# Performance work log

Hardware: AMD Instinct MI355X
Metric: run time of the kernel (lower is better)

Reference implementation:

```python
import jax, jax.numpy as jnp
import numpy as np

B, S, D, H = 2, 2048, 1024, 16
DH = D // H
DFF = 4 * D
EPS = 1e-5
NEG = -1e9


def _layernorm(x, gamma, beta):
    mu = jnp.mean(x, axis=-1, keepdims=True)
    var = jnp.mean(jnp.square(x - mu), axis=-1, keepdims=True)
    return (x - mu) * jax.lax.rsqrt(var + EPS) * gamma + beta


def setup_inputs() -> dict:
    key = jax.random.key(0)
    ks = jax.random.split(key, 12)
    s = 0.02
    X = jax.random.normal(ks[0], (B, S, D), dtype=jnp.float32)
    # causal mask (True = attend)
    attention_mask = jnp.tril(jnp.ones((S, S), dtype=bool))
    return {
        "X": X,
        "attention_mask": attention_mask,
        "gamma1": jnp.ones((D,), jnp.float32),
        "beta1": jnp.zeros((D,), jnp.float32),
        "Wq": jax.random.normal(ks[1], (H, D, DH), jnp.float32) * s,
        "bq": jnp.zeros((H, DH), jnp.float32),
        "Wk": jax.random.normal(ks[2], (H, D, DH), jnp.float32) * s,
        "bk": jnp.zeros((H, DH), jnp.float32),
        "Wv": jax.random.normal(ks[3], (H, D, DH), jnp.float32) * s,
        "bv": jnp.zeros((H, DH), jnp.float32),
        "W0": jax.random.normal(ks[4], (D, D), jnp.float32) * s,
        "b0": jnp.zeros((D,), jnp.float32),
        "gamma2": jnp.ones((D,), jnp.float32),
        "beta2": jnp.zeros((D,), jnp.float32),
        "W1": jax.random.normal(ks[5], (D, DFF), jnp.float32) * s,
        "b1": jnp.zeros((DFF,), jnp.float32),
        "W2": jax.random.normal(ks[6], (DFF, D), jnp.float32) * s,
        "b2": jnp.zeros((D,), jnp.float32),
    }


def reference(X, attention_mask, gamma1, beta1, Wq, bq, Wk, bk, Wv, bv, W0, b0,
              gamma2, beta2, W1, b1, W2, b2):
    scale = 1.0 / np.sqrt(DH)
    # --- pre-LN MHA ---
    Xn = _layernorm(X, gamma1, beta1)
    # per-head projections, stacked: [B,H,S,DH]
    Q = jnp.einsum('bsd,hdk->bhsk', Xn, Wq) + bq[None, :, None, :]
    K = jnp.einsum('bsd,hdk->bhsk', Xn, Wk) + bk[None, :, None, :]
    V = jnp.einsum('bsd,hdk->bhsk', Xn, Wv) + bv[None, :, None, :]
    scores = jnp.einsum('bhsk,bhtk->bhst', Q, K) * scale
    scores = jnp.where(attention_mask, scores, NEG)
    weights = jax.nn.softmax(scores, axis=-1)
    attn = jnp.einsum('bhst,bhtv->bhsv', weights, V)  # [B,H,S,DH]
    # concat heads (head-major along feature dim, matching torch.cat order)
    attn = attn.transpose(0, 2, 1, 3).reshape(B, S, D)
    mha = attn @ W0 + b0
    X = mha + X  # residual (dropout = identity at eval)
    # --- pre-LN FFN ---
    Xn2 = _layernorm(X, gamma2, beta2)
    h = jax.nn.relu(Xn2 @ W1 + b1)
    ffn = h @ W2 + b2
    return ffn + X
```

## Files before the change

### kernel.cpp

```cpp
#include <hip/hip_runtime.h>
#include <hip/hip_bf16.h>

#define BB 2
#define SS 2048
#define DDIM 1024
#define HH 16
#define DHH 64
#define DFF_ 4096
#define BS 4096
#define NQKV 3072

typedef unsigned short u16;
using short8  = __attribute__((ext_vector_type(8))) short;
using floatx4 = __attribute__((ext_vector_type(4))) float;
using ushort4_t = __attribute__((ext_vector_type(4))) unsigned short;

__device__ __forceinline__ u16 f2b(float f){
  union { unsigned int u; float f; } v; v.f = f;
  unsigned int u = v.u;
  u += 0x7FFFu + ((u >> 16) & 1u);
  return (u16)(u >> 16);
}

__device__ __forceinline__ void gl2lds16(const u16* g, u16* l){
  __builtin_amdgcn_global_load_lds((const __attribute__((address_space(1))) void*)g,
                                   (__attribute__((address_space(3))) void*)l, 16, 0, 0);
}

__device__ __forceinline__ void ln_row(const float* __restrict__ x,
                                       const float* __restrict__ gamma,
                                       const float* __restrict__ beta,
                                       u16* __restrict__ y, int row, float* smem){
  const float4* xr = (const float4*)(x + (size_t)row * DDIM);
  int tid = threadIdx.x;
  float4 v = xr[tid];
  float s  = v.x + v.y + v.z + v.w;
  float ss = v.x*v.x + v.y*v.y + v.z*v.z + v.w*v.w;
  for (int o = 1; o < 64; o <<= 1){ s += __shfl_xor(s, o, 64); ss += __shfl_xor(ss, o, 64); }
  int wid = tid >> 6;
  if ((tid & 63) == 0){ smem[wid] = s; smem[wid + 4] = ss; }
  __syncthreads();
  s  = smem[0] + smem[1] + smem[2] + smem[3];
  ss = smem[4] + smem[5] + smem[6] + smem[7];
  float mu  = s / (float)DDIM;
  float var = ss / (float)DDIM - mu * mu;
  float rs  = rsqrtf(var + 1e-5f);
  const float4* gp = (const float4*)gamma;
  const float4* bp = (const float4*)beta;
  float4 g = gp[tid], b = bp[tid];
  u16* yr = y + (size_t)row * DDIM + tid*4;
  yr[0] = f2b((v.x - mu) * rs * g.x + b.x);
  yr[1] = f2b((v.y - mu) * rs * g.y + b.y);
  yr[2] = f2b((v.z - mu) * rs * g.z + b.z);
  yr[3] = f2b((v.w - mu) * rs * g.w + b.w);
}

__device__ __forceinline__ void tcast(const float* __restrict__ in, u16* __restrict__ out,
                                      int R, int C, int tile, float (*sh)[33]){
  int nr = R >> 5;
  int tr = tile % nr, tc = tile / nr;
  int r0 = tr * 32, c0 = tc * 32;
  int tx = threadIdx.x & 31, ty = threadIdx.x >> 5;
  for (int i = ty; i < 32; i += 8)
    sh[i][tx] = in[(size_t)(r0 + i) * C + c0 + tx];
  __syncthreads();
  for (int i = ty; i < 32; i += 8)
    out[(size_t)(c0 + i) * R + r0 + tx] = f2b(sh[tx][i]);
}

__global__ __launch_bounds__(256) void prep_ln1_k(
    const float* __restrict__ X, const float* __restrict__ g1, const float* __restrict__ be1,
    u16* __restrict__ Xn,
    const float* __restrict__ Wq, const float* __restrict__ Wk, const float* __restrict__ Wv,
    const float* __restrict__ W0, const float* __restrict__ W1,
    const float* __restrict__ bq, const float* __restrict__ bk, const float* __restrict__ bv,
    u16* __restrict__ wqkvT, u16* __restrict__ w0T, u16* __restrict__ w1T,
    float* __restrict__ biasQKV)
{
  __shared__ float sh[32][33];
  __shared__ float smem8[8];
  int id = blockIdx.x;
  if (id < 4096){
    ln_row(X, g1, be1, Xn, id, smem8);
  } else if (id < 7168){
    int lid2 = id - 4096;
    int which = lid2 >> 10, lid = lid2 & 1023;
    const float* src = which == 0 ? Wq : (which == 1 ? Wk : Wv);
    u16* dst = wqkvT + (size_t)which * 1048576;
    int bat = lid >> 6, t = lid & 63;
    tcast(src + (size_t)bat * 65536, dst + (size_t)bat * 65536, 1024, 64, t, sh);
  } else if (id < 8192){
    tcast(W0, w0T, 1024, 1024, id - 7168, sh);
  } else if (id < 12288){
    tcast(W1, w1T, 1024, 4096, id - 8192, sh);
  } else {
    int idx = (id - 12288) * 256 + threadIdx.x;
    if (idx < 3072){
      float v = idx < 1024 ? bq[idx] : (idx < 2048 ? bk[idx - 1024] : bv[idx - 2048]);
      biasQKV[idx] = v;
    }
  }
}

__global__ __launch_bounds__(256) void w2t_ln2_k(
    const float* __restrict__ X1, const float* __restrict__ g2, const float* __restrict__ be2,
    u16* __restrict__ Xn2, const float* __restrict__ W2, u16* __restrict__ w2T)
{
  __shared__ float sh[32][33];
  __shared__ float smem8[8];
  int id = blockIdx.x;
  if (id < 4096){
    ln_row(X1, g2, be2, Xn2, id, smem8);
  } else {
    int tile = id - 4096;
    int tr = tile / 32, tc = tile % 32;
    int r0 = tr * 32, c0 = tc * 32;
    int tx = threadIdx.x & 31, ty = threadIdx.x >> 5;
    for (int i = ty; i < 32; i += 8)
      sh[i][tx] = W2[(size_t)(r0 + i) * 1024 + c0 + tx];
    __syncthreads();
    for (int i = ty; i < 32; i += 8)
      w2T[(size_t)(c0 + i) * 4096 + r0 + tx] = f2b(sh[tx][i]);
  }
}

__global__ __launch_bounds__(256) void vt_k(const u16* __restrict__ QKV, u16* __restrict__ VT){
  __shared__ u16 t[32][33];
  int bh = blockIdx.z; int b = bh >> 4, h = bh & 15;
  int s0 = blockIdx.x * 32, d0 = blockIdx.y * 32;
  int tx = threadIdx.x & 31, ty = threadIdx.x >> 5;
  const u16* src = QKV + (size_t)b * SS * NQKV + 2048 + h * DHH;
  for (int i = ty; i < 32; i += 8)
    t[i][tx] = src[(size_t)(s0 + i) * NQKV + d0 + tx];
  __syncthreads();
  u16* dst = VT + (size_t)bh * DHH * SS;
  for (int i = ty; i < 32; i += 8)
    dst[(size_t)(d0 + i) * SS + s0 + tx] = t[tx][i];
}

template<int TM, int TN>
__global__ __launch_bounds__(256) void gemm_db(
    const u16* __restrict__ A, const u16* __restrict__ Bt,
    const float* __restrict__ bias, const float* __restrict__ res,
    void* __restrict__ Cv, int M, int N, int K, int relu, int writeBf16)
{
  constexpr int ACH = TM / 16;
  constexpr int BCH = TN / 16;
  constexpr int CH1 = ACH + BCH;
  constexpr int CPW = (2 * CH1) / 4;
  constexpr int MI  = TM / 32;
  constexpr int NI  = TN / 32;

  __shared__ __align__(16) u16 As[2][2][TM * 32];
  __shared__ __align__(16) u16 Bs[2][2][TN * 32];

  int tid  = threadIdx.x;
  int wave = tid >> 6, lane = tid & 63;
  int quad = lane >> 4, l16 = lane & 15;

  int gx = gridDim.x, gy = gridDim.y;
  int bid = blockIdx.x + gx * blockIdx.y;
  int xcd = bid & 7, idx = bid >> 3;
  int by  = xcd * (gy >> 3) + idx / gx;
  int bx  = idx % gx;

  int m0 = by * TM, n0 = bx * TN;
  int wm = (wave >> 1) * (TM / 2), wn = (wave & 1) * (TN / 2);

  floatx4 acc[MI][NI] = {};

  int srow = lane >> 2;
  int scol = (lane & 3) * 8;
  const u16* gptr[CPW]; u16* lp0[CPW]; int lstep[CPW];
#pragma unroll
  for (int k = 0; k < CPW; k++){
    int c = wave * CPW + k;
    int p = c / CH1, cc = c % CH1;
    if (cc < ACH){
      gptr[k]  = A + (size_t)(m0 + cc*16 + srow) * K + p*32 + scol;
      lp0[k]   = &As[0][p][cc * 512];
      lstep[k] = 2 * TM * 32;
    } else {
      gptr[k]  = Bt + (size_t)(n0 + (cc-ACH)*16 + srow) * K + p*32 + scol;
      lp0[k]   = &Bs[0][p][(cc-ACH) * 512];
      lstep[k] = 2 * TN * 32;
    }
  }

  int nsteps = K >> 6;

#pragma unroll
  for (int k = 0; k < CPW; k++){ gl2lds16(gptr[k], lp0[k]); gptr[k] += 64; }
  asm volatile("s_waitcnt vmcnt(0)" ::: "memory");
  __builtin_amdgcn_sched_barrier(0);
  __builtin_amdgcn_s_barrier();
  __builtin_amdgcn_sched_barrier(0);

  for (int t = 0; t < nsteps; ++t){
    int cur = t & 1;
    if (t + 1 < nsteps){
#pragma unroll
      for (int k = 0; k < CPW; k++){
        gl2lds16(gptr[k], lp0[k] + (cur ? 0 : lstep[k]));
        gptr[k] += 64;
      }
    }
    __builtin_amdgcn_s_setprio(1);
#pragma unroll
    for (int p = 0; p < 2; p++){
      short8 af[MI], bf[NI];
#pragma unroll
      for (int i = 0; i < MI; i++)
        af[i] = *(short8*)&As[cur][p][(wm + i*16 + l16)*32 + quad*8];
#pragma unroll
      for (int j = 0; j < NI; j++)
        bf[j] = *(short8*)&Bs[cur][p][(wn + j*16 + l16)*32 + quad*8];
#pragma unroll
      for (int i = 0; i < MI; i++)
#pragma unroll
        for (int j = 0; j < NI; j++)
          acc[i][j] = __builtin_amdgcn_mfma_f32_16x16x32_bf16(bf[j], af[i], acc[i][j], 0,0,0);
    }
    __builtin_amdgcn_s_setprio(0);
    if (t + 1 < nsteps){
      asm volatile("s_waitcnt vmcnt(0)" ::: "memory");
      __builtin_amdgcn_sched_barrier(0);
      __builtin_amdgcn_s_barrier();
      __builtin_amdgcn_sched_barrier(0);
    }
  }

  u16*   Cb = (u16*)Cv;
  float* Cf = (float*)Cv;
#pragma unroll
  for (int i = 0; i < MI; i++){
    int row = m0 + wm + i*16 + l16;
#pragma unroll
    for (int j = 0; j < NI; j++){
      int col = n0 + wn + j*16 + quad*4;
      float v0 = acc[i][j][0], v1 = acc[i][j][1], v2 = acc[i][j][2], v3 = acc[i][j][3];
      if (bias){
        const float4 bb = *(const float4*)&bias[col];
        v0 += bb.x; v1 += bb.y; v2 += bb.z; v3 += bb.w;
      }
      if (relu){
        v0 = v0 > 0.f ? v0 : 0.f; v1 = v1 > 0.f ? v1 : 0.f;
        v2 = v2 > 0.f ? v2 : 0.f; v3 = v3 > 0.f ? v3 : 0.f;
      }
      if (res){
        const float4 rr = *(const float4*)&res[(size_t)row * N + col];
        v0 += rr.x; v1 += rr.y; v2 += rr.z; v3 += rr.w;
      }
      if (writeBf16){
        ushort4_t o = { f2b(v0), f2b(v1), f2b(v2), f2b(v3) };
        *(ushort4_t*)&Cb[(size_t)row * N + col] = o;
      } else {
        float4 o; o.x = v0; o.y = v1; o.z = v2; o.w = v3;
        *(float4*)&Cf[(size_t)row * N + col] = o;
      }
    }
  }
}

#define KT   128
#define KsLD 72
#define VTLD 136
#define PsLD 136

__global__ __launch_bounds__(256) void attn_k(
    const u16* __restrict__ QKV, const u16* __restrict__ VT, u16* __restrict__ O)
{
  int bh = blockIdx.x;
  int b = bh >> 4, h = bh & 15;
  int qt = (int)gridDim.y - 1 - blockIdx.y;
  int q0 = qt * 64;
  const u16* Qb_  = QKV + (size_t)b * SS * NQKV + h * DHH;
  const u16* Kb_  = Qb_ + 1024;
  const u16* VTb_ = VT + (size_t)bh * DHH * SS;

  __shared__ __align__(16) u16 Ks [KT * KsLD];
  __shared__ __align__(16) u16 VTs[DHH * VTLD];
  __shared__ __align__(16) u16 Ps [4][16 * PsLD];

  int tid = threadIdx.x;
  int wave = tid >> 6, lane = tid & 63;
  int quad = lane >> 4, l16 = lane & 15;
  int qrow = q0 + wave * 16;

  short8 qf0, qf1;
  {
    const u16* qp = Qb_ + (size_t)(qrow + l16) * NQKV + quad*8;
    qf0 = *(const short8*)qp;
    qf1 = *(const short8*)(qp + 32);
  }

  float l_acc[4] = {0.f, 0.f, 0.f, 0.f};
  floatx4 oacc[4] = {};

  int nk = (qt >> 1) + 1;
  int lim = wave + 4 * (qt & 1);
  const float qs = 0.125f * 1.44269504088896f;

  short8 kreg[4], vreg[4];
#pragma unroll
  for (int it = 0; it < 4; it++){
    int g = tid + it * 256;
    kreg[it] = *(const short8*)(Kb_ + (size_t)(g >> 3) * NQKV + (g & 7) * 8);
    vreg[it] = *(const short8*)(VTb_ + (size_t)(g >> 4) * SS + (g & 15) * 8);
  }

  for (int kt = 0; kt < nk; kt++){
    int k0 = kt * KT;
    __syncthreads();
#pragma unroll
    for (int it = 0; it < 4; it++){
      int g = tid + it * 256;
      *(short8*)&Ks [(g >> 3) * KsLD + (g & 7) * 8]  = kreg[it];
      *(short8*)&VTs[(g >> 4) * VTLD + (g & 15) * 8] = vreg[it];
    }
    __syncthreads();

    if (kt + 1 < nk){
      int kn = k0 + KT;
#pragma unroll
      for (int it = 0; it < 4; it++){
        int g = tid + it * 256;
        kreg[it] = *(const short8*)(Kb_ + (size_t)(kn + (g >> 3)) * NQKV + (g & 7) * 8);
        vreg[it] = *(const short8*)(VTb_ + (size_t)(g >> 4) * SS + kn + (g & 15) * 8);
      }
    }

    bool last = (kt == nk - 1);
    int stmax = last ? lim : 7;
    floatx4 sacc[8] = {};
    __builtin_amdgcn_s_setprio(1);
#pragma unroll
    for (int st = 0; st < 8; st++){
      if (st <= stmax){
        short8 kb0 = *(short8*)&Ks[(st*16 + l16) * KsLD + quad*8];
        short8 kb1 = *(short8*)&Ks[(st*16 + l16) * KsLD + 32 + quad*8];
        sacc[st] = __builtin_amdgcn_mfma_f32_16x16x32_bf16(qf0, kb0, sacc[st], 0,0,0);
        sacc[st] = __builtin_amdgcn_mfma_f32_16x16x32_bf16(qf1, kb1, sacc[st], 0,0,0);
      }
    }
    __builtin_amdgcn_s_setprio(0);

#pragma unroll
    for (int st = 0; st < 8; st++){
      if (st <= stmax){
        if (last){
          int col = k0 + st*16 + l16;
#pragma unroll
          for (int r = 0; r < 4; r++){
            float e = exp2f(sacc[st][r] * qs);
            e = (col <= qrow + quad*4 + r) ? e : 0.f;
            l_acc[r] += e;
            Ps[wave][(quad*4 + r) * PsLD + st*16 + l16] = f2b(e);
          }
        } else {
#pragma unroll
          for (int r = 0; r < 4; r++){
            float e = exp2f(sacc[st][r] * qs);
            l_acc[r] += e;
            Ps[wave][(quad*4 + r) * PsLD + st*16 + l16] = f2b(e);
          }
        }
      } else {
#pragma unroll
        for (int r = 0; r < 4; r++)
          Ps[wave][(quad*4 + r) * PsLD + st*16 + l16] = 0;
      }
    }
    asm volatile("s_waitcnt lgkmcnt(0)" ::: "memory");

    int cmax = last ? (lim >> 1) : 3;
    short8 pa[4];
#pragma unroll
    for (int c = 0; c < 4; c++)
      pa[c] = *(short8*)&Ps[wave][l16 * PsLD + c*32 + quad*8];
    __builtin_amdgcn_s_setprio(1);
#pragma unroll
    for (int ost = 0; ost < 4; ost++){
#pragma unroll
      for (int c = 0; c < 4; c++){
        if (c <= cmax){
          short8 vb = *(short8*)&VTs[(ost*16 + l16) * VTLD + c*32 + quad*8];
          oacc[ost] = __builtin_amdgcn_mfma_f32_16x16x32_bf16(pa[c], vb, oacc[ost], 0,0,0);
        }
      }
    }
    __builtin_amdgcn_s_setprio(0);
  }

#pragma unroll
  for (int r = 0; r < 4; r++){
    for (int o = 1; o < 16; o <<= 1) l_acc[r] += __shfl_xor(l_acc[r], o, 64);
  }
  float inv[4];
#pragma unroll
  for (int r = 0; r < 4; r++) inv[r] = 1.0f / l_acc[r];

#pragma unroll
  for (int ost = 0; ost < 4; ost++)
#pragma unroll
    for (int r = 0; r < 4; r++){
      int s  = qrow + quad*4 + r;
      int dh = ost*16 + l16;
      O[((size_t)b * SS + s) * DDIM + h * DHH + dh] = f2b(oacc[ost][r] * inv[r]);
    }
}

extern "C" void kernel_launch(void* const* d_in, const int* in_sizes, int n_in,
                              void* d_out, int out_size, void* d_ws, size_t ws_size,
                              hipStream_t stream) {
  const float* X   = (const float*)d_in[0];
  const float* g1  = (const float*)d_in[2];
  const float* be1 = (const float*)d_in[3];
  const float* Wq  = (const float*)d_in[4];
  const float* bq  = (const float*)d_in[5];
  const float* Wk  = (const float*)d_in[6];
  const float* bk  = (const float*)d_in[7];
  const float* Wv  = (const float*)d_in[8];
  const float* bv  = (const float*)d_in[9];
  const float* W0  = (const float*)d_in[10];
  const float* b0  = (const float*)d_in[11];
  const float* g2  = (const float*)d_in[12];
  const float* be2 = (const float*)d_in[13];
  const float* W1  = (const float*)d_in[14];
  const float* b1  = (const float*)d_in[15];
  const float* W2  = (const float*)d_in[16];
  const float* b2  = (const float*)d_in[17];
  float* out = (float*)d_out;

  u16* ws16 = (u16*)d_ws;
  u16* wqkvT = ws16;
  u16* w0T   = ws16 + 3145728;
  u16* w2T   = ws16;
  u16* w1T   = ws16 + 4194304;
  u16* QKVb  = ws16 + 8388608;
  u16* VTb   = ws16 + 8388608 + 12582912;
  u16* hb    = ws16 + 8388608;
  u16* Xn    = ws16 + 25165824;
  u16* attnB = Xn;
  float* biasQKV = (float*)(ws16 + 29360128);

  prep_ln1_k<<<dim3(12300), 256, 0, stream>>>(X, g1, be1, Xn,
      Wq, Wk, Wv, W0, W1, bq, bk, bv, wqkvT, w0T, w1T, biasQKV);

  gemm_db<128,128><<<dim3(24, 32), 256, 0, stream>>>(Xn, wqkvT, biasQKV, nullptr, QKVb,
      BS, NQKV, 1024, 0, 1);

  vt_k<<<dim3(64, 2, 32), 256, 0, stream>>>(QKVb, VTb);

  attn_k<<<dim3(32, 32), 256, 0, stream>>>(QKVb, VTb, attnB);

  gemm_db<64,128><<<dim3(8, 64), 256, 0, stream>>>(attnB, w0T, b0, X, out,
      BS, DDIM, 1024, 0, 0);

  w2t_ln2_k<<<dim3(8192), 256, 0, stream>>>(out, g2, be2, Xn, W2, w2T);

  gemm_db<128,128><<<dim3(32, 32), 256, 0, stream>>>(Xn, w1T, b1, nullptr, hb,
      BS, DFF_, 1024, 1, 1);
  gemm_db<64,128><<<dim3(8, 64), 256, 0, stream>>>(hb, w2T, b2, out, out,
      BS, DDIM, DFF_, 0, 0);
}
```

Measured before the change: 370.2 us.

## Process 128 query rows per attention block to reuse K/V tiles

Each attention block now handles two 64-row query groups per wave pair (128 rows), sharing each staged K and V^T tile across both groups, and the grid is halved. This cuts global K/V loads and LDS staging per query row. In exchange, register pressure from doubled score and output accumulators rises, and fewer blocks with uneven causal work may reduce occupancy and load balance.

```diff
diff --git a/kernel.cpp b/kernel.cpp
--- a/kernel.cpp
+++ b/kernel.cpp
@@ -273,7 +273,7 @@
   int bh = blockIdx.x;
   int b = bh >> 4, h = bh & 15;
   int qt = (int)gridDim.y - 1 - blockIdx.y;
-  int q0 = qt * 64;
+  int q0 = qt * 128;
   const u16* Qb_  = QKV + (size_t)b * SS * NQKV + h * DHH;
   const u16* Kb_  = Qb_ + 1024;
   const u16* VTb_ = VT + (size_t)bh * DHH * SS;
@@ -285,20 +285,25 @@
   int tid = threadIdx.x;
   int wave = tid >> 6, lane = tid & 63;
   int quad = lane >> 4, l16 = lane & 15;
-  int qrow = q0 + wave * 16;
-
-  short8 qf0, qf1;
+  int qrow0 = q0 + wave * 16;
+  int qrow1 = qrow0 + 64;
+
+  short8 qf0a, qf0b, qf1a, qf1b;
   {
-    const u16* qp = Qb_ + (size_t)(qrow + l16) * NQKV + quad*8;
-    qf0 = *(const short8*)qp;
-    qf1 = *(const short8*)(qp + 32);
-  }
-
-  float l_acc[4] = {0.f, 0.f, 0.f, 0.f};
-  floatx4 oacc[4] = {};
-
-  int nk = (qt >> 1) + 1;
-  int lim = wave + 4 * (qt & 1);
+    const u16* qp0 = Qb_ + (size_t)(qrow0 + l16) * NQKV + quad*8;
+    qf0a = *(const short8*)qp0;
+    qf0b = *(const short8*)(qp0 + 32);
+    const u16* qp1 = Qb_ + (size_t)(qrow1 + l16) * NQKV + quad*8;
+    qf1a = *(const short8*)qp1;
+    qf1b = *(const short8*)(qp1 + 32);
+  }
+
+  float l0[4] = {0.f,0.f,0.f,0.f}, l1[4] = {0.f,0.f,0.f,0.f};
+  floatx4 oa0[4] = {}, oa1[4] = {};
+
+  int nk = qt + 1;
+  int lim0 = wave;
+  int lim1 = wave + 4;
   const float qs = 0.125f * 1.44269504088896f;
 
   short8 kreg[4], vreg[4];
@@ -331,37 +336,43 @@
     }
 
     bool last = (kt == nk - 1);
-    int stmax = last ? lim : 7;
-    floatx4 sacc[8] = {};
+    int s0max = last ? lim0 : 7;
+    int s1max = last ? lim1 : 7;
+
+    floatx4 sacc0[8] = {}, sacc1[8] = {};
     __builtin_amdgcn_s_setprio(1);
 #pragma unroll
     for (int st = 0; st < 8; st++){
-      if (st <= stmax){
+      if (st <= s1max){
         short8 kb0 = *(short8*)&Ks[(st*16 + l16) * KsLD + quad*8];
         short8 kb1 = *(short8*)&Ks[(st*16 + l16) * KsLD + 32 + quad*8];
-        sacc[st] = __builtin_amdgcn_mfma_f32_16x16x32_bf16(qf0, kb0, sacc[st], 0,0,0);
-        sacc[st] = __builtin_amdgcn_mfma_f32_16x16x32_bf16(qf1, kb1, sacc[st], 0,0,0);
+        if (st <= s0max){
+          sacc0[st] = __builtin_amdgcn_mfma_f32_16x16x32_bf16(qf0a, kb0, sacc0[st], 0,0,0);
+          sacc0[st] = __builtin_amdgcn_mfma_f32_16x16x32_bf16(qf0b, kb1, sacc0[st], 0,0,0);
+        }
+        sacc1[st] = __builtin_amdgcn_mfma_f32_16x16x32_bf16(qf1a, kb0, sacc1[st], 0,0,0);
+        sacc1[st] = __builtin_amdgcn_mfma_f32_16x16x32_bf16(qf1b, kb1, sacc1[st], 0,0,0);
       }
     }
     __builtin_amdgcn_s_setprio(0);
 
 #pragma unroll
     for (int st = 0; st < 8; st++){
-      if (st <= stmax){
+      if (st <= s0max){
         if (last){
           int col = k0 + st*16 + l16;
 #pragma unroll
           for (int r = 0; r < 4; r++){
-            float e = exp2f(sacc[st][r] * qs);
-            e = (col <= qrow + quad*4 + r) ? e : 0.f;
-            l_acc[r] += e;
+            float e = exp2f(sacc0[st][r] * qs);
+            e = (col <= qrow0 + quad*4 + r) ? e : 0.f;
+            l0[r] += e;
             Ps[wave][(quad*4 + r) * PsLD + st*16 + l16] = f2b(e);
           }
         } else {
 #pragma unroll
           for (int r = 0; r < 4; r++){
-            float e = exp2f(sacc[st][r] * qs);
-            l_acc[r] += e;
+            float e = exp2f(sacc0[st][r] * qs);
+            l0[r] += e;
             Ps[wave][(quad*4 + r) * PsLD + st*16 + l16] = f2b(e);
           }
         }
@@ -373,40 +384,95 @@
     }
     asm volatile("s_waitcnt lgkmcnt(0)" ::: "memory");
 
-    int cmax = last ? (lim >> 1) : 3;
-    short8 pa[4];
-#pragma unroll
-    for (int c = 0; c < 4; c++)
-      pa[c] = *(short8*)&Ps[wave][l16 * PsLD + c*32 + quad*8];
-    __builtin_amdgcn_s_setprio(1);
-#pragma unroll
-    for (int ost = 0; ost < 4; ost++){
-#pragma unroll
-      for (int c = 0; c < 4; c++){
-        if (c <= cmax){
-          short8 vb = *(short8*)&VTs[(ost*16 + l16) * VTLD + c*32 + quad*8];
-          oacc[ost] = __builtin_amdgcn_mfma_f32_16x16x32_bf16(pa[c], vb, oacc[ost], 0,0,0);
+    {
+      int cmax = last ? (lim0 >> 1) : 3;
+      short8 pa[4];
+#pragma unroll
+      for (int c = 0; c < 4; c++)
+        pa[c] = *(short8*)&Ps[wave][l16 * PsLD + c*32 + quad*8];
+      __builtin_amdgcn_s_setprio(1);
+#pragma unroll
+      for (int ost = 0; ost < 4; ost++){
+#pragma unroll
+        for (int c = 0; c < 4; c++){
+          if (c <= cmax){
+            short8 vb = *(short8*)&VTs[(ost*16 + l16) * VTLD + c*32 + quad*8];
+            oa0[ost] = __builtin_amdgcn_mfma_f32_16x16x32_bf16(pa[c], vb, oa0[ost], 0,0,0);
+          }
         }
       }
-    }
-    __builtin_amdgcn_s_setprio(0);
+      __builtin_amdgcn_s_setprio(0);
+    }
+
+#pragma unroll
+    for (int st = 0; st < 8; st++){
+      if (st <= s1max){
+        if (last){
+          int col = k0 + st*16 + l16;
+#pragma unroll
+          for (int r = 0; r < 4; r++){
+            float e = exp2f(sacc1[st][r] * qs);
+            e = (col <= qrow1 + quad*4 + r) ? e : 0.f;
+            l1[r] += e;
+            Ps[wave][(quad*4 + r) * PsLD + st*16 + l16] = f2b(e);
+          }
+        } else {
+#pragma unroll
+          for (int r = 0; r < 4; r++){
+            float e = exp2f(sacc1[st][r] * qs);
+            l1[r] += e;
+            Ps[wave][(quad*4 + r) * PsLD + st*16 + l16] = f2b(e);
+          }
+        }
+      } else {
+#pragma unroll
+        for (int r = 0; r < 4; r++)
+          Ps[wave][(quad*4 + r) * PsLD + st*16 + l16] = 0;
+      }
+    }
+    asm volatile("s_waitcnt lgkmcnt(0)" ::: "memory");
+
+    {
+      int cmax = last ? (lim1 >> 1) : 3;
+      short8 pa[4];
+#pragma unroll
+      for (int c = 0; c < 4; c++)
+        pa[c] = *(short8*)&Ps[wave][l16 * PsLD + c*32 + quad*8];
+      __builtin_amdgcn_s_setprio(1);
+#pragma unroll
+      for (int ost = 0; ost < 4; ost++){
+#pragma unroll
+        for (int c = 0; c < 4; c++){
+          if (c <= cmax){
+            short8 vb = *(short8*)&VTs[(ost*16 + l16) * VTLD + c*32 + quad*8];
+            oa1[ost] = __builtin_amdgcn_mfma_f32_16x16x32_bf16(pa[c], vb, oa1[ost], 0,0,0);
+          }
+        }
+      }
+      __builtin_amdgcn_s_setprio(0);
+    }
   }
 
 #pragma unroll
   for (int r = 0; r < 4; r++){
-    for (int o = 1; o < 16; o <<= 1) l_acc[r] += __shfl_xor(l_acc[r], o, 64);
-  }
-  float inv[4];
-#pragma unroll
-  for (int r = 0; r < 4; r++) inv[r] = 1.0f / l_acc[r];
+    for (int o = 1; o < 16; o <<= 1){
+      l0[r] += __shfl_xor(l0[r], o, 64);
+      l1[r] += __shfl_xor(l1[r], o, 64);
+    }
+  }
+  float inv0[4], inv1[4];
+#pragma unroll
+  for (int r = 0; r < 4; r++){ inv0[r] = 1.0f / l0[r]; inv1[r] = 1.0f / l1[r]; }
 
 #pragma unroll
   for (int ost = 0; ost < 4; ost++)
 #pragma unroll
     for (int r = 0; r < 4; r++){
-      int s  = qrow + quad*4 + r;
       int dh = ost*16 + l16;
-      O[((size_t)b * SS + s) * DDIM + h * DHH + dh] = f2b(oacc[ost][r] * inv[r]);
+      int s0r = qrow0 + quad*4 + r;
+      int s1r = qrow1 + quad*4 + r;
+      O[((size_t)b * SS + s0r) * DDIM + h * DHH + dh] = f2b(oa0[ost][r] * inv0[r]);
+      O[((size_t)b * SS + s1r) * DDIM + h * DHH + dh] = f2b(oa1[ost][r] * inv1[r]);
     }
 }
 
@@ -452,7 +518,7 @@
 
   vt_k<<<dim3(64, 2, 32), 256, 0, stream>>>(QKVb, VTb);
 
-  attn_k<<<dim3(32, 32), 256, 0, stream>>>(QKVb, VTb, attnB);
+  attn_k<<<dim3(32, 16), 256, 0, stream>>>(QKVb, VTb, attnB);
 
   gemm_db<64,128><<<dim3(8, 64), 256, 0, stream>>>(attnB, w0T, b0, X, out,
       BS, DDIM, 1024, 0, 0);
```

After: 411.8 us. +11.2%, slower.

## Double attention block to 128 query rows and swizzle LDS layouts

Applied to the files above, without the earlier changes.

The attention kernel now runs 512 threads (8 waves) per block covering 128 query rows instead of 64. Each K/V tile loaded into LDS is therefore shared by twice as many waves, halving the number of blocks and the per-block global loads. The padded LDS strides are replaced with XOR-swizzled unpadded layouts for K, V^T and P, meant to avoid bank conflicts. The trade-off is fewer blocks in the grid, so the causal load imbalance per block gets coarser.

```diff
diff --git a/kernel.cpp b/kernel.cpp
--- a/kernel.cpp
+++ b/kernel.cpp
@@ -262,30 +262,27 @@
   }
 }
 
-#define KT   128
-#define KsLD 72
-#define VTLD 136
-#define PsLD 136
-
-__global__ __launch_bounds__(256) void attn_k(
+#define KT 128
+
+__global__ __launch_bounds__(512) void attn_k(
     const u16* __restrict__ QKV, const u16* __restrict__ VT, u16* __restrict__ O)
 {
   int bh = blockIdx.x;
   int b = bh >> 4, h = bh & 15;
-  int qt = (int)gridDim.y - 1 - blockIdx.y;
-  int q0 = qt * 64;
+  int t  = (int)gridDim.y - 1 - blockIdx.y;
   const u16* Qb_  = QKV + (size_t)b * SS * NQKV + h * DHH;
   const u16* Kb_  = Qb_ + 1024;
   const u16* VTb_ = VT + (size_t)bh * DHH * SS;
 
-  __shared__ __align__(16) u16 Ks [KT * KsLD];
-  __shared__ __align__(16) u16 VTs[DHH * VTLD];
-  __shared__ __align__(16) u16 Ps [4][16 * PsLD];
+  __shared__ __align__(16) u16 Ks [KT * 64];
+  __shared__ __align__(16) u16 VTs[DHH * 128];
+  __shared__ __align__(16) u16 Ps [8][16 * 128];
 
   int tid = threadIdx.x;
   int wave = tid >> 6, lane = tid & 63;
+  int g = wave >> 2, w = wave & 3;
   int quad = lane >> 4, l16 = lane & 15;
-  int qrow = q0 + wave * 16;
+  int qrow = t * 128 + g * 64 + w * 16;
 
   short8 qf0, qf1;
   {
@@ -297,36 +294,38 @@
   float l_acc[4] = {0.f, 0.f, 0.f, 0.f};
   floatx4 oacc[4] = {};
 
-  int nk = (qt >> 1) + 1;
-  int lim = wave + 4 * (qt & 1);
+  int nk = t + 1;
+  int lim = w + 4 * g;
   const float qs = 0.125f * 1.44269504088896f;
 
-  short8 kreg[4], vreg[4];
-#pragma unroll
-  for (int it = 0; it < 4; it++){
-    int g = tid + it * 256;
-    kreg[it] = *(const short8*)(Kb_ + (size_t)(g >> 3) * NQKV + (g & 7) * 8);
-    vreg[it] = *(const short8*)(VTb_ + (size_t)(g >> 4) * SS + (g & 15) * 8);
+  short8 kreg[2], vreg[2];
+#pragma unroll
+  for (int it = 0; it < 2; it++){
+    int gg = tid + it * 512;
+    kreg[it] = *(const short8*)(Kb_ + (size_t)(gg >> 3) * NQKV + (gg & 7) * 8);
+    vreg[it] = *(const short8*)(VTb_ + (size_t)(gg >> 4) * SS + (gg & 15) * 8);
   }
 
   for (int kt = 0; kt < nk; kt++){
     int k0 = kt * KT;
     __syncthreads();
 #pragma unroll
-    for (int it = 0; it < 4; it++){
-      int g = tid + it * 256;
-      *(short8*)&Ks [(g >> 3) * KsLD + (g & 7) * 8]  = kreg[it];
-      *(short8*)&VTs[(g >> 4) * VTLD + (g & 15) * 8] = vreg[it];
+    for (int it = 0; it < 2; it++){
+      int gg = tid + it * 512;
+      { int row = gg >> 3, idx = (row * 64 + (gg & 7) * 8) ^ ((row & 7) << 3);
+        *(short8*)&Ks[idx] = kreg[it]; }
+      { int row = gg >> 4, idx = (row * 128 + (gg & 15) * 8) ^ ((row & 7) << 3);
+        *(short8*)&VTs[idx] = vreg[it]; }
     }
     __syncthreads();
 
     if (kt + 1 < nk){
       int kn = k0 + KT;
 #pragma unroll
-      for (int it = 0; it < 4; it++){
-        int g = tid + it * 256;
-        kreg[it] = *(const short8*)(Kb_ + (size_t)(kn + (g >> 3)) * NQKV + (g & 7) * 8);
-        vreg[it] = *(const short8*)(VTb_ + (size_t)(g >> 4) * SS + kn + (g & 15) * 8);
+      for (int it = 0; it < 2; it++){
+        int gg = tid + it * 512;
+        kreg[it] = *(const short8*)(Kb_ + (size_t)(kn + (gg >> 3)) * NQKV + (gg & 7) * 8);
+        vreg[it] = *(const short8*)(VTb_ + (size_t)(gg >> 4) * SS + kn + (gg & 15) * 8);
       }
     }
 
@@ -337,8 +336,10 @@
 #pragma unroll
     for (int st = 0; st < 8; st++){
       if (st <= stmax){
-        short8 kb0 = *(short8*)&Ks[(st*16 + l16) * KsLD + quad*8];
-        short8 kb1 = *(short8*)&Ks[(st*16 + l16) * KsLD + 32 + quad*8];
+        int r0i = (st*16 + l16) * 64;
+        int sw  = (l16 & 7) << 3;
+        short8 kb0 = *(short8*)&Ks[(r0i + quad*8) ^ sw];
+        short8 kb1 = *(short8*)&Ks[(r0i + 32 + quad*8) ^ sw];
         sacc[st] = __builtin_amdgcn_mfma_f32_16x16x32_bf16(qf0, kb0, sacc[st], 0,0,0);
         sacc[st] = __builtin_amdgcn_mfma_f32_16x16x32_bf16(qf1, kb1, sacc[st], 0,0,0);
       }
@@ -355,20 +356,24 @@
             float e = exp2f(sacc[st][r] * qs);
             e = (col <= qrow + quad*4 + r) ? e : 0.f;
             l_acc[r] += e;
-            Ps[wave][(quad*4 + r) * PsLD + st*16 + l16] = f2b(e);
+            int row = quad*4 + r;
+            Ps[wave][(row * 128 + st*16 + l16) ^ ((row & 7) << 3)] = f2b(e);
           }
         } else {
 #pragma unroll
           for (int r = 0; r < 4; r++){
             float e = exp2f(sacc[st][r] * qs);
             l_acc[r] += e;
-            Ps[wave][(quad*4 + r) * PsLD + st*16 + l16] = f2b(e);
+            int row = quad*4 + r;
+            Ps[wave][(row * 128 + st*16 + l16) ^ ((row & 7) << 3)] = f2b(e);
           }
         }
       } else {
 #pragma unroll
-        for (int r = 0; r < 4; r++)
-          Ps[wave][(quad*4 + r) * PsLD + st*16 + l16] = 0;
+        for (int r = 0; r < 4; r++){
+          int row = quad*4 + r;
+          Ps[wave][(row * 128 + st*16 + l16) ^ ((row & 7) << 3)] = 0;
+        }
       }
     }
     asm volatile("s_waitcnt lgkmcnt(0)" ::: "memory");
@@ -377,14 +382,14 @@
     short8 pa[4];
 #pragma unroll
     for (int c = 0; c < 4; c++)
-      pa[c] = *(short8*)&Ps[wave][l16 * PsLD + c*32 + quad*8];
+      pa[c] = *(short8*)&Ps[wave][(l16 * 128 + c*32 + quad*8) ^ ((l16 & 7) << 3)];
     __builtin_amdgcn_s_setprio(1);
 #pragma unroll
     for (int ost = 0; ost < 4; ost++){
 #pragma unroll
       for (int c = 0; c < 4; c++){
         if (c <= cmax){
-          short8 vb = *(short8*)&VTs[(ost*16 + l16) * VTLD + c*32 + quad*8];
+          short8 vb = *(short8*)&VTs[((ost*16 + l16) * 128 + c*32 + quad*8) ^ ((l16 & 7) << 3)];
           oacc[ost] = __builtin_amdgcn_mfma_f32_16x16x32_bf16(pa[c], vb, oacc[ost], 0,0,0);
         }
       }
@@ -452,7 +457,7 @@
 
   vt_k<<<dim3(64, 2, 32), 256, 0, stream>>>(QKVb, VTb);
 
-  attn_k<<<dim3(32, 32), 256, 0, stream>>>(QKVb, VTb, attnB);
+  attn_k<<<dim3(32, 16), 512, 0, stream>>>(QKVb, VTb, attnB);
 
   gemm_db<64,128><<<dim3(8, 64), 256, 0, stream>>>(attnB, w0T, b0, X, out,
       BS, DDIM, 1024, 0, 0);
```

After: 368.4 us. No clear change (-0.5%).
